# Optimization experiments

Hardware: AMD Instinct MI355X
Metric: run time of the kernel (lower is better)

The kernel has to match this reference:

```python
import jax, jax.numpy as jnp
import numpy as np

B, N, C = 1, 256, 128        # batch, n_res, norm_channel
H, AC = 4, 32                # num_head, attention_channel


def setup_inputs() -> dict:
    key = jax.random.key(0)
    ks = jax.random.split(key, 9)
    s = 0.02
    return {
        "act": jax.random.normal(ks[0], (B, N, N, C), jnp.float32),
        "mask": jnp.ones((B, N, N), jnp.float32),
        "ln_g": jnp.ones((C,), jnp.float32),
        "ln_b": jnp.zeros((C,), jnp.float32),
        "wq": (jax.random.normal(ks[1], (C, H * AC), jnp.float32) * s),
        "wk": (jax.random.normal(ks[2], (C, H * AC), jnp.float32) * s),
        "wv": (jax.random.normal(ks[3], (C, H * AC), jnp.float32) * s),
        "w2d": (jax.random.normal(ks[4], (C, H), jnp.float32) * s),
        "wg": (jax.random.normal(ks[5], (C, H * AC), jnp.float32) * s),
        "bg": jnp.zeros((H * AC,), jnp.float32),
        "wo": (jax.random.normal(ks[6], (H * AC, C), jnp.float32) * s),
        "bo": jnp.zeros((C,), jnp.float32),
    }


def reference(act, mask, ln_g, ln_b, wq, wk, wv, w2d, wg, bg, wo, bo):
    eps = 1e-5
    mu = jnp.mean(act, axis=-1, keepdims=True)
    var = jnp.mean(jnp.square(act - mu), axis=-1, keepdims=True)
    a = (act - mu) * jax.lax.rsqrt(var + eps) * ln_g + ln_b  # LayerNorm

    b_, m_, i_, _ = a.shape
    q = (a @ wq).reshape(b_, m_, i_, H, AC)
    k = (a @ wk).reshape(b_, m_, i_, H, AC)
    v = (a @ wv).reshape(b_, m_, i_, H, AC)

    factor = 1.0 / np.sqrt(AC).astype(np.float32)
    # mask bias: [b, m, 1, 1, j]
    bias = (1e9 * (mask - 1.0))[:, :, None, None, :]
    aff = jnp.einsum('bmihc,bmjhc->bmhij', q * factor, k) + bias

    # pair bias: [b, h, i, j], broadcast over m (torch trailing-dim broadcast, b=1)
    nb = jnp.einsum('bijc,ch->bhij', a, w2d)
    weights = jax.nn.softmax(aff + nb[:, None], axis=-1)  # [b,m,h,i,j]

    g = jax.nn.sigmoid(a @ wg + bg).reshape(b_, m_, i_, H, AC)
    out = jnp.einsum('bmhqk,bmkhc->bmqhc', weights, v) * g  # [b,m,q,h,c]
    return out.reshape(b_, m_, i_, H * AC) @ wo + bo
```

## Files before the change

### kernel.cpp

```cpp
#include <hip/hip_runtime.h>
#include <hip/hip_fp16.h>
#include <math.h>


#define NRES 256
#define CCH  128
#define NROWS (NRES * NRES)
#define FACTOR 0.17677669529663687f
#define LOG2E  1.44269504088896341f

typedef __attribute__((ext_vector_type(8))) __bf16 bf16x8;
typedef __attribute__((ext_vector_type(4))) float f32x4;

__device__ __forceinline__ f32x4 mfma16(bf16x8 a, bf16x8 b, f32x4 c) {
    return __builtin_amdgcn_mfma_f32_16x16x32_bf16(a, b, c, 0, 0, 0);
}

union PK4 { __bf16 b[4]; uint2 u2; };

__device__ __forceinline__ void hilo(float x, __bf16& h, __bf16& l) {
    h = (__bf16)x;
    l = (__bf16)(x - (float)h);
}

__global__ __launch_bounds__(256) void pre_kernel(
    const float* __restrict__ act, const float* __restrict__ ln_g,
    const float* __restrict__ ln_b, const float* __restrict__ w2d,
    const float* __restrict__ wq, const float* __restrict__ wk,
    const float* __restrict__ wv, const float* __restrict__ wg,
    const float* __restrict__ wo,
    __bf16* __restrict__ wph, __bf16* __restrict__ wpl,
    float* __restrict__ nbP, __bf16* __restrict__ aLN)
{
    const int t = threadIdx.x;
    if (blockIdx.x >= 2048) {
        const int gid = (blockIdx.x - 2048) * 256 + t;
        const int wid = gid >> 11;
        const int rem = gid & 2047;
        const int nstrip = rem >> 8;
        const int kf = (rem >> 6) & 3;
        const int lane = rem & 63;
        const int l15 = lane & 15, quad = lane >> 4;
        const float* W = (wid == 0) ? wq : (wid == 1) ? wk :
                         (wid == 2) ? wv : (wid == 3) ? wg : wo;
        const float scale = (wid == 0) ? FACTOR * LOG2E : 1.0f;
        bf16x8 hb, lb;
        #pragma unroll
        for (int e = 0; e < 8; ++e) {
            int k = kf * 32 + quad * 8 + e;
            int n = nstrip * 16 + l15;
            float v = W[k * CCH + n] * scale;
            __bf16 h, l; hilo(v, h, l);
            hb[e] = h; lb[e] = l;
        }
        *(bf16x8*)&wph[(size_t)gid * 8] = hb;
        *(bf16x8*)&wpl[(size_t)gid * 8] = lb;
        return;
    }
    const int ridx = t >> 3, g = t & 7;
    const int grow = blockIdx.x * 32 + ridx;
    const float* __restrict__ xp = act + (size_t)grow * CCH + g * 16;
    float4 x4[4];
    #pragma unroll
    for (int c = 0; c < 4; ++c) x4[c] = *(const float4*)(xp + c * 4);
    float s = 0.f, sq = 0.f;
    #pragma unroll
    for (int c = 0; c < 4; ++c) {
        s  += (x4[c].x + x4[c].y) + (x4[c].z + x4[c].w);
        sq += x4[c].x * x4[c].x + x4[c].y * x4[c].y +
              x4[c].z * x4[c].z + x4[c].w * x4[c].w;
    }
    #pragma unroll
    for (int o = 1; o <= 4; o <<= 1) {
        s  += __shfl_xor(s, o, 64);
        sq += __shfl_xor(sq, o, 64);
    }
    float mu  = s * (1.0f / CCH);
    float var = fmaf(sq, 1.0f / CCH, -mu * mu);
    float rs  = rsqrtf(var + 1e-5f);
    float av[16];
    #pragma unroll
    for (int c = 0; c < 4; ++c) {
        float4 g4 = *(const float4*)&ln_g[g * 16 + c * 4];
        float4 b4 = *(const float4*)&ln_b[g * 16 + c * 4];
        float* xv = (float*)&x4[c];
        float* gv = (float*)&g4;
        float* bv = (float*)&b4;
        #pragma unroll
        for (int e = 0; e < 4; ++e)
            av[c * 4 + e] = fmaf((xv[e] - mu) * rs, gv[e], bv[e]);
    }
    bf16x8 o1, o2;
    #pragma unroll
    for (int e = 0; e < 8; ++e) {
        o1[e] = (__bf16)av[e];
        o2[e] = (__bf16)av[8 + e];
    }
    *(bf16x8*)&aLN[(size_t)grow * CCH + g * 16] = o1;
    *(bf16x8*)&aLN[(size_t)grow * CCH + g * 16 + 8] = o2;

    float nb[4] = {0.f, 0.f, 0.f, 0.f};
    const float4* __restrict__ w2d4 = (const float4*)w2d;
    #pragma unroll
    for (int c = 0; c < 16; ++c) {
        float4 wv = w2d4[g * 16 + c];
        nb[0] = fmaf(av[c], wv.x, nb[0]);
        nb[1] = fmaf(av[c], wv.y, nb[1]);
        nb[2] = fmaf(av[c], wv.z, nb[2]);
        nb[3] = fmaf(av[c], wv.w, nb[3]);
    }
    #pragma unroll
    for (int o = 1; o <= 4; o <<= 1)
        #pragma unroll
        for (int hh = 0; hh < 4; ++hh)
            nb[hh] += __shfl_xor(nb[hh], o, 64);
    if (g == 0) {
        const int i = grow >> 8, j = grow & 255;
        #pragma unroll
        for (int hh = 0; hh < 4; ++hh) {
            size_t f = ((size_t)hh << 14) + ((size_t)(i >> 4) << 10) +
                       ((size_t)(j >> 4) << 6) + ((size_t)((j >> 2) & 3) << 4) +
                       (i & 15);
            nbP[f * 4 + (j & 3)] = nb[hh] * LOG2E;
        }
    }
}

__device__ __forceinline__ void proj16(const bf16x8* A0,
    const __bf16* __restrict__ Bh, int lane, f32x4* acc)
{
    #pragma unroll
    for (int n = 0; n < 8; ++n) acc[n] = (f32x4){0.f, 0.f, 0.f, 0.f};
    #pragma unroll
    for (int kf = 0; kf < 4; ++kf)
        #pragma unroll
        for (int n = 0; n < 8; ++n) {
            bf16x8 bh = *(const bf16x8*)&Bh[(size_t)((n * 4 + kf) * 64 + lane) * 8];
            acc[n] = mfma16(A0[kf], bh, acc[n]);
        }
}

__global__ __launch_bounds__(1024) void mega_kernel(
    const __bf16* __restrict__ aLN, const __bf16* __restrict__ wph,
    const __bf16* __restrict__ wpl, const float* __restrict__ bg,
    const float* __restrict__ mask, const float* __restrict__ nbP,
    const float* __restrict__ bo, float* __restrict__ out)
{
    __shared__ __align__(16) char smem[158720];
    const int t = threadIdx.x, w = t >> 6, lane = t & 63;
    const int l15 = lane & 15, quad = lane >> 4;
    const int m = blockIdx.x;
    __bf16* const Kl = (__bf16*)smem;
    __bf16* const aH = (__bf16*)(smem + w * 4352);
    __bf16* const VT = (__bf16*)(smem + 69632);
    __bf16* const ph = (__bf16*)(smem + 137216 + w * 1280);
    float*  const biasrow = (float*)(smem + 157696);

    if (t < 256)
        biasrow[t] = fmaf(1.442695e9f, mask[m * NRES + t] - 1.0f, -4.0f * LOG2E);

    bf16x8 A0[4];
    {
        const __bf16* __restrict__ ap =
            aLN + ((size_t)m * NRES + w * 16 + l15) * CCH;
        #pragma unroll
        for (int kf = 0; kf < 4; ++kf)
            A0[kf] = *(const bf16x8*)&ap[kf * 32 + quad * 8];
    }

    f32x4 acc[8];
    bf16x8 Qh[4];
    uint2  greg[4][2];

    proj16(A0, wph, lane, acc);
    {
        __bf16* const sth = aH;
        #pragma unroll
        for (int n = 0; n < 8; ++n)
            #pragma unroll
            for (int r = 0; r < 4; ++r)
                sth[(quad * 4 + r) * 136 + n * 16 + l15] = (__bf16)acc[n][r];
        #pragma unroll
        for (int h = 0; h < 4; ++h)
            Qh[h] = *(const bf16x8*)&sth[l15 * 136 + h * 32 + quad * 8];
    }

    proj16(A0, wph + 3 * 16384, lane, acc);
    {
        __half* const sthH = (__half*)aH;
        #pragma unroll
        for (int n = 0; n < 8; ++n)
            #pragma unroll
            for (int r = 0; r < 4; ++r) {
                float v = acc[n][r] + bg[n * 16 + l15];
                sthH[(quad * 4 + r) * 136 + n * 16 + l15] =
                    (__half)(1.0f / (1.0f + __expf(-v)));
            }
        #pragma unroll
        for (int h = 0; h < 4; ++h)
            #pragma unroll
            for (int c = 0; c < 2; ++c)
                greg[h][c] =
                    *(const uint2*)&sthH[l15 * 136 + h * 32 + c * 16 + quad * 4];
    }

    proj16(A0, wph + 1 * 16384, lane, acc);
    #pragma unroll
    for (int n = 0; n < 8; ++n)
        #pragma unroll
        for (int r = 0; r < 4; ++r)
            aH[(quad * 4 + r) * 136 + n * 16 + l15] = (__bf16)acc[n][r];

    proj16(A0, wph + 2 * 16384, lane, acc);
    {
        const int jcol = w * 16 + quad * 4;
        #pragma unroll
        for (int n = 0; n < 8; ++n) {
            PK4 pv;
            #pragma unroll
            for (int r = 0; r < 4; ++r) pv.b[r] = (__bf16)acc[n][r];
            *(uint2*)&VT[(n * 16 + l15) * 264 + jcol] = pv.u2;
        }
    }

    __syncthreads();

    uint2 ovh[4][2], ovl[4][2];
    #pragma unroll
    for (int h = 0; h < 4; ++h) {
        f32x4 O[2];
        O[0] = (f32x4){0.f, 0.f, 0.f, 0.f};
        O[1] = (f32x4){0.f, 0.f, 0.f, 0.f};
        float ls = 0.f;
        const int nbbase = (h * 16384 + w * 1024 + quad * 16 + l15) * 4;
        float4 nb_a[2], nb_b[2];
        #pragma unroll
        for (int js = 0; js < 2; ++js)
            nb_a[js] = *(const float4*)(nbP + nbbase + (js << 8));
        #pragma unroll 1
        for (int jb = 0; jb < NRES; jb += 32) {
            bf16x8 Kh[2];
            #pragma unroll
            for (int js = 0; js < 2; ++js)
                Kh[js] = *(const bf16x8*)&Kl[(jb + js * 16 + l15) * 136 +
                                             h * 32 + quad * 8];
            bf16x8 Vh2[2];
            #pragma unroll
            for (int c = 0; c < 2; ++c)
                Vh2[c] = *(const bf16x8*)&VT[(h * 32 + c * 16 + l15) * 264 +
                                             jb + quad * 8];
            const int jn = (jb + 32 < NRES) ? (jb >> 4) + 2 : 0;
            #pragma unroll
            for (int js = 0; js < 2; ++js)
                nb_b[js] = *(const float4*)(nbP + nbbase + ((jn + js) << 8));
            #pragma unroll
            for (int js = 0; js < 2; ++js) {
                f32x4 S = (f32x4){0.f, 0.f, 0.f, 0.f};
                S = mfma16(Kh[js], Qh[h], S);
                float4 nb4 = nb_a[js];
                float4 mb4 = *(const float4*)&biasrow[jb + js * 16 + quad * 4];
                float p0 = exp2f(S[0] + nb4.x + mb4.x);
                float p1 = exp2f(S[1] + nb4.y + mb4.y);
                float p2 = exp2f(S[2] + nb4.z + mb4.z);
                float p3 = exp2f(S[3] + nb4.w + mb4.w);
                ls += (p0 + p1) + (p2 + p3);
                PK4 hh;
                hh.b[0] = (__bf16)p0; hh.b[1] = (__bf16)p1;
                hh.b[2] = (__bf16)p2; hh.b[3] = (__bf16)p3;
                *(uint2*)&ph[l15 * 40 + js * 16 + quad * 4] = hh.u2;
            }
            bf16x8 Ph = *(const bf16x8*)&ph[l15 * 40 + quad * 8];
            #pragma unroll
            for (int c = 0; c < 2; ++c)
                O[c] = mfma16(Vh2[c], Ph, O[c]);
            nb_a[0] = nb_b[0];
            nb_a[1] = nb_b[1];
        }
        ls += __shfl_xor(ls, 16, 64);
        ls += __shfl_xor(ls, 32, 64);
        float inv = 1.0f / ls;
        #pragma unroll
        for (int c = 0; c < 2; ++c) {
            const __half* gh = (const __half*)&greg[h][c];
            PK4 hh, lo;
            #pragma unroll
            for (int r = 0; r < 4; ++r) {
                float v = O[c][r] * inv * (float)gh[r];
                __bf16 hb; __bf16 lb; hilo(v, hb, lb);
                hh.b[r] = hb; lo.b[r] = lb;
            }
            ovh[h][c] = hh.u2;
            ovl[h][c] = lo.u2;
        }
    }
    __syncthreads();

    {
        __bf16* const sth = aH;
        #pragma unroll
        for (int h = 0; h < 4; ++h)
            #pragma unroll
            for (int c = 0; c < 2; ++c)
                *(uint2*)&sth[l15 * 136 + h * 32 + c * 16 + quad * 4] = ovh[h][c];
        bf16x8 Ah0[4];
        #pragma unroll
        for (int kf = 0; kf < 4; ++kf)
            Ah0[kf] = *(const bf16x8*)&sth[l15 * 136 + kf * 32 + quad * 8];
        #pragma unroll
        for (int h = 0; h < 4; ++h)
            #pragma unroll
            for (int c = 0; c < 2; ++c)
                *(uint2*)&sth[l15 * 136 + h * 32 + c * 16 + quad * 4] = ovl[h][c];
        bf16x8 Al0[4];
        #pragma unroll
        for (int kf = 0; kf < 4; ++kf)
            Al0[kf] = *(const bf16x8*)&sth[l15 * 136 + kf * 32 + quad * 8];

        const __bf16* __restrict__ Bh = wph + (size_t)4 * 16384;
        const __bf16* __restrict__ Bl = wpl + (size_t)4 * 16384;
        #pragma unroll
        for (int n = 0; n < 8; ++n) acc[n] = (f32x4){0.f, 0.f, 0.f, 0.f};
        #pragma unroll
        for (int kf = 0; kf < 4; ++kf)
            #pragma unroll
            for (int n = 0; n < 8; ++n) {
                size_t boff = (size_t)((n * 4 + kf) * 64 + lane) * 8;
                bf16x8 bh = *(const bf16x8*)&Bh[boff];
                bf16x8 bl = *(const bf16x8*)&Bl[boff];
                acc[n] = mfma16(Ah0[kf], bh, acc[n]);
                acc[n] = mfma16(Ah0[kf], bl, acc[n]);
                acc[n] = mfma16(Al0[kf], bh, acc[n]);
            }

        const size_t rbase = (size_t)m * NRES + w * 16;
        #pragma unroll
        for (int n = 0; n < 8; ++n) {
            float b = bo[n * 16 + l15];
            #pragma unroll
            for (int r = 0; r < 4; ++r)
                out[(rbase + quad * 4 + r) * CCH + n * 16 + l15] = acc[n][r] + b;
        }
    }
}

extern "C" void kernel_launch(void* const* d_in, const int* in_sizes, int n_in,
                              void* d_out, int out_size, void* d_ws, size_t ws_size,
                              hipStream_t stream)
{
    const float* act  = (const float*)d_in[0];
    const float* mask = (const float*)d_in[1];
    const float* ln_g = (const float*)d_in[2];
    const float* ln_b = (const float*)d_in[3];
    const float* wq   = (const float*)d_in[4];
    const float* wk   = (const float*)d_in[5];
    const float* wv   = (const float*)d_in[6];
    const float* w2d  = (const float*)d_in[7];
    const float* wg   = (const float*)d_in[8];
    const float* bg   = (const float*)d_in[9];
    const float* wo   = (const float*)d_in[10];
    const float* bo   = (const float*)d_in[11];
    float* out = (float*)d_out;

    float* nbP = (float*)d_ws;
    __bf16* wph = (__bf16*)(nbP + 4 * NROWS);
    __bf16* wpl = wph + 5 * 16384;
    __bf16* aLN = wpl + 5 * 16384;

    pre_kernel<<<2088, 256, 0, stream>>>(
        act, ln_g, ln_b, w2d, wq, wk, wv, wg, wo, wph, wpl, nbP, aLN);
    mega_kernel<<<256, 1024, 0, stream>>>(
        aLN, wph, wpl, bg, mask, nbP, bo, out);
}
```

Before: 189.0 us.

## Use 16x16x16 MFMA to feed accumulators directly, removing LDS round-trips

Switches the PV product and the output projection to the 16x16x16 bf16 MFMA. That instruction's operand layout matches the accumulator layout of the previous MFMA, so probabilities and attention outputs can be fed straight from registers. This removes the per-iteration P staging through shared memory, the final __syncthreads, and the LDS transposes before the wo projection. It also drops the unused low-part weights for q/k/v/g and repacks wo for the new layout. In exchange it issues twice as many smaller MFMAs and more, narrower global loads of the weights.

```diff
diff --git a/kernel.cpp b/kernel.cpp
--- a/kernel.cpp
+++ b/kernel.cpp
@@ -11,12 +11,16 @@
 
 typedef __attribute__((ext_vector_type(8))) __bf16 bf16x8;
 typedef __attribute__((ext_vector_type(4))) float f32x4;
+typedef __attribute__((ext_vector_type(4))) short s16x4;
 
 __device__ __forceinline__ f32x4 mfma16(bf16x8 a, bf16x8 b, f32x4 c) {
     return __builtin_amdgcn_mfma_f32_16x16x32_bf16(a, b, c, 0, 0, 0);
 }
-
-union PK4 { __bf16 b[4]; uint2 u2; };
+__device__ __forceinline__ f32x4 mfma16x16(s16x4 a, s16x4 b, f32x4 c) {
+    return __builtin_amdgcn_mfma_f32_16x16x16bf16_1k(a, b, c, 0, 0, 0);
+}
+
+union PK4 { __bf16 b[4]; uint2 u2; s16x4 s4; };
 
 __device__ __forceinline__ void hilo(float x, __bf16& h, __bf16& l) {
     h = (__bf16)x;
@@ -29,7 +33,8 @@
     const float* __restrict__ wq, const float* __restrict__ wk,
     const float* __restrict__ wv, const float* __restrict__ wg,
     const float* __restrict__ wo,
-    __bf16* __restrict__ wph, __bf16* __restrict__ wpl,
+    __bf16* __restrict__ wph, __bf16* __restrict__ wo16h,
+    __bf16* __restrict__ wo16l,
     float* __restrict__ nbP, __bf16* __restrict__ aLN)
 {
     const int t = threadIdx.x;
@@ -37,24 +42,41 @@
         const int gid = (blockIdx.x - 2048) * 256 + t;
         const int wid = gid >> 11;
         const int rem = gid & 2047;
-        const int nstrip = rem >> 8;
-        const int kf = (rem >> 6) & 3;
         const int lane = rem & 63;
         const int l15 = lane & 15, quad = lane >> 4;
-        const float* W = (wid == 0) ? wq : (wid == 1) ? wk :
-                         (wid == 2) ? wv : (wid == 3) ? wg : wo;
-        const float scale = (wid == 0) ? FACTOR * LOG2E : 1.0f;
-        bf16x8 hb, lb;
-        #pragma unroll
-        for (int e = 0; e < 8; ++e) {
-            int k = kf * 32 + quad * 8 + e;
-            int n = nstrip * 16 + l15;
-            float v = W[k * CCH + n] * scale;
-            __bf16 h, l; hilo(v, h, l);
-            hb[e] = h; lb[e] = l;
-        }
-        *(bf16x8*)&wph[(size_t)gid * 8] = hb;
-        *(bf16x8*)&wpl[(size_t)gid * 8] = lb;
+        if (wid < 4) {
+            const int nstrip = rem >> 8;
+            const int kf = (rem >> 6) & 3;
+            const float* W = (wid == 0) ? wq : (wid == 1) ? wk :
+                             (wid == 2) ? wv : wg;
+            const float scale = (wid == 0) ? FACTOR * LOG2E : 1.0f;
+            bf16x8 hb;
+            #pragma unroll
+            for (int e = 0; e < 8; ++e) {
+                int k = kf * 32 + quad * 8 + e;
+                int n = nstrip * 16 + l15;
+                hb[e] = (__bf16)(W[k * CCH + n] * scale);
+            }
+            *(bf16x8*)&wph[(size_t)gid * 8] = hb;
+        } else {
+            const int nstrip = rem >> 8;
+            const int kcp = (rem >> 6) & 3;
+            #pragma unroll
+            for (int sub = 0; sub < 2; ++sub) {
+                const int kc = kcp * 2 + sub;
+                PK4 hh, ll;
+                #pragma unroll
+                for (int e = 0; e < 4; ++e) {
+                    int k = kc * 16 + quad * 4 + e;
+                    int n = nstrip * 16 + l15;
+                    __bf16 h, l; hilo(wo[k * CCH + n], h, l);
+                    hh.b[e] = h; ll.b[e] = l;
+                }
+                const int fo = ((nstrip * 8 + kc) * 64 + lane) * 4;
+                *(uint2*)&wo16h[fo] = hh.u2;
+                *(uint2*)&wo16l[fo] = ll.u2;
+            }
+        }
         return;
     }
     const int ridx = t >> 3, g = t & 7;
@@ -142,19 +164,19 @@
 
 __global__ __launch_bounds__(1024) void mega_kernel(
     const __bf16* __restrict__ aLN, const __bf16* __restrict__ wph,
-    const __bf16* __restrict__ wpl, const float* __restrict__ bg,
-    const float* __restrict__ mask, const float* __restrict__ nbP,
-    const float* __restrict__ bo, float* __restrict__ out)
+    const __bf16* __restrict__ wo16h, const __bf16* __restrict__ wo16l,
+    const float* __restrict__ bg, const float* __restrict__ mask,
+    const float* __restrict__ nbP, const float* __restrict__ bo,
+    float* __restrict__ out)
 {
-    __shared__ __align__(16) char smem[158720];
+    __shared__ __align__(16) char smem[138240];
     const int t = threadIdx.x, w = t >> 6, lane = t & 63;
     const int l15 = lane & 15, quad = lane >> 4;
     const int m = blockIdx.x;
     __bf16* const Kl = (__bf16*)smem;
     __bf16* const aH = (__bf16*)(smem + w * 4352);
     __bf16* const VT = (__bf16*)(smem + 69632);
-    __bf16* const ph = (__bf16*)(smem + 137216 + w * 1280);
-    float*  const biasrow = (float*)(smem + 157696);
+    float*  const biasrow = (float*)(smem + 137216);
 
     if (t < 256)
         biasrow[t] = fmaf(1.442695e9f, mask[m * NRES + t] - 1.0f, -4.0f * LOG2E);
@@ -225,7 +247,7 @@
 
     __syncthreads();
 
-    uint2 ovh[4][2], ovl[4][2];
+    PK4 ovh[4][2], ovl[4][2];
     #pragma unroll
     for (int h = 0; h < 4; ++h) {
         f32x4 O[2];
@@ -244,35 +266,47 @@
             for (int js = 0; js < 2; ++js)
                 Kh[js] = *(const bf16x8*)&Kl[(jb + js * 16 + l15) * 136 +
                                              h * 32 + quad * 8];
-            bf16x8 Vh2[2];
+            PK4 Vf[2][2];
             #pragma unroll
             for (int c = 0; c < 2; ++c)
-                Vh2[c] = *(const bf16x8*)&VT[(h * 32 + c * 16 + l15) * 264 +
-                                             jb + quad * 8];
+                #pragma unroll
+                for (int js = 0; js < 2; ++js)
+                    Vf[c][js].u2 = *(const uint2*)&VT[
+                        (h * 32 + c * 16 + l15) * 264 + jb + js * 16 + quad * 4];
             const int jn = (jb + 32 < NRES) ? (jb >> 4) + 2 : 0;
             #pragma unroll
             for (int js = 0; js < 2; ++js)
                 nb_b[js] = *(const float4*)(nbP + nbbase + ((jn + js) << 8));
-            #pragma unroll
-            for (int js = 0; js < 2; ++js) {
-                f32x4 S = (f32x4){0.f, 0.f, 0.f, 0.f};
-                S = mfma16(Kh[js], Qh[h], S);
-                float4 nb4 = nb_a[js];
-                float4 mb4 = *(const float4*)&biasrow[jb + js * 16 + quad * 4];
-                float p0 = exp2f(S[0] + nb4.x + mb4.x);
-                float p1 = exp2f(S[1] + nb4.y + mb4.y);
-                float p2 = exp2f(S[2] + nb4.z + mb4.z);
-                float p3 = exp2f(S[3] + nb4.w + mb4.w);
+            f32x4 S0 = (f32x4){0.f, 0.f, 0.f, 0.f};
+            f32x4 S1 = (f32x4){0.f, 0.f, 0.f, 0.f};
+            S0 = mfma16(Kh[0], Qh[h], S0);
+            S1 = mfma16(Kh[1], Qh[h], S1);
+            PK4 PJ0, PJ1;
+            {
+                float4 mb0 = *(const float4*)&biasrow[jb + quad * 4];
+                float p0 = exp2f(S0[0] + nb_a[0].x + mb0.x);
+                float p1 = exp2f(S0[1] + nb_a[0].y + mb0.y);
+                float p2 = exp2f(S0[2] + nb_a[0].z + mb0.z);
+                float p3 = exp2f(S0[3] + nb_a[0].w + mb0.w);
                 ls += (p0 + p1) + (p2 + p3);
-                PK4 hh;
-                hh.b[0] = (__bf16)p0; hh.b[1] = (__bf16)p1;
-                hh.b[2] = (__bf16)p2; hh.b[3] = (__bf16)p3;
-                *(uint2*)&ph[l15 * 40 + js * 16 + quad * 4] = hh.u2;
-            }
-            bf16x8 Ph = *(const bf16x8*)&ph[l15 * 40 + quad * 8];
-            #pragma unroll
-            for (int c = 0; c < 2; ++c)
-                O[c] = mfma16(Vh2[c], Ph, O[c]);
+                PJ0.b[0] = (__bf16)p0; PJ0.b[1] = (__bf16)p1;
+                PJ0.b[2] = (__bf16)p2; PJ0.b[3] = (__bf16)p3;
+            }
+            {
+                float4 mb1 = *(const float4*)&biasrow[jb + 16 + quad * 4];
+                float p0 = exp2f(S1[0] + nb_a[1].x + mb1.x);
+                float p1 = exp2f(S1[1] + nb_a[1].y + mb1.y);
+                float p2 = exp2f(S1[2] + nb_a[1].z + mb1.z);
+                float p3 = exp2f(S1[3] + nb_a[1].w + mb1.w);
+                ls += (p0 + p1) + (p2 + p3);
+                PJ1.b[0] = (__bf16)p0; PJ1.b[1] = (__bf16)p1;
+                PJ1.b[2] = (__bf16)p2; PJ1.b[3] = (__bf16)p3;
+            }
+            #pragma unroll
+            for (int c = 0; c < 2; ++c) {
+                O[c] = mfma16x16(Vf[c][0].s4, PJ0.s4, O[c]);
+                O[c] = mfma16x16(Vf[c][1].s4, PJ1.s4, O[c]);
+            }
             nb_a[0] = nb_b[0];
             nb_a[1] = nb_b[1];
         }
@@ -282,55 +316,34 @@
         #pragma unroll
         for (int c = 0; c < 2; ++c) {
             const __half* gh = (const __half*)&greg[h][c];
-            PK4 hh, lo;
             #pragma unroll
             for (int r = 0; r < 4; ++r) {
                 float v = O[c][r] * inv * (float)gh[r];
                 __bf16 hb; __bf16 lb; hilo(v, hb, lb);
-                hh.b[r] = hb; lo.b[r] = lb;
-            }
-            ovh[h][c] = hh.u2;
-            ovl[h][c] = lo.u2;
-        }
-    }
-    __syncthreads();
-
-    {
-        __bf16* const sth = aH;
-        #pragma unroll
-        for (int h = 0; h < 4; ++h)
-            #pragma unroll
-            for (int c = 0; c < 2; ++c)
-                *(uint2*)&sth[l15 * 136 + h * 32 + c * 16 + quad * 4] = ovh[h][c];
-        bf16x8 Ah0[4];
-        #pragma unroll
-        for (int kf = 0; kf < 4; ++kf)
-            Ah0[kf] = *(const bf16x8*)&sth[l15 * 136 + kf * 32 + quad * 8];
-        #pragma unroll
-        for (int h = 0; h < 4; ++h)
-            #pragma unroll
-            for (int c = 0; c < 2; ++c)
-                *(uint2*)&sth[l15 * 136 + h * 32 + c * 16 + quad * 4] = ovl[h][c];
-        bf16x8 Al0[4];
-        #pragma unroll
-        for (int kf = 0; kf < 4; ++kf)
-            Al0[kf] = *(const bf16x8*)&sth[l15 * 136 + kf * 32 + quad * 8];
-
-        const __bf16* __restrict__ Bh = wph + (size_t)4 * 16384;
-        const __bf16* __restrict__ Bl = wpl + (size_t)4 * 16384;
+                ovh[h][c].b[r] = hb; ovl[h][c].b[r] = lb;
+            }
+        }
+    }
+
+    {
         #pragma unroll
         for (int n = 0; n < 8; ++n) acc[n] = (f32x4){0.f, 0.f, 0.f, 0.f};
         #pragma unroll
-        for (int kf = 0; kf < 4; ++kf)
+        for (int kc = 0; kc < 8; ++kc) {
+            const int h = kc >> 1, c = kc & 1;
+            s16x4 Ah = ovh[h][c].s4;
+            s16x4 Al = ovl[h][c].s4;
             #pragma unroll
             for (int n = 0; n < 8; ++n) {
-                size_t boff = (size_t)((n * 4 + kf) * 64 + lane) * 8;
-                bf16x8 bh = *(const bf16x8*)&Bh[boff];
-                bf16x8 bl = *(const bf16x8*)&Bl[boff];
-                acc[n] = mfma16(Ah0[kf], bh, acc[n]);
-                acc[n] = mfma16(Ah0[kf], bl, acc[n]);
-                acc[n] = mfma16(Al0[kf], bh, acc[n]);
-            }
+                const int fo = ((n * 8 + kc) * 64 + lane) * 4;
+                PK4 bh, bl;
+                bh.u2 = *(const uint2*)&wo16h[fo];
+                bl.u2 = *(const uint2*)&wo16l[fo];
+                acc[n] = mfma16x16(Ah, bh.s4, acc[n]);
+                acc[n] = mfma16x16(Ah, bl.s4, acc[n]);
+                acc[n] = mfma16x16(Al, bh.s4, acc[n]);
+            }
+        }
 
         const size_t rbase = (size_t)m * NRES + w * 16;
         #pragma unroll
@@ -361,13 +374,14 @@
     const float* bo   = (const float*)d_in[11];
     float* out = (float*)d_out;
 
-    float* nbP = (float*)d_ws;
-    __bf16* wph = (__bf16*)(nbP + 4 * NROWS);
-    __bf16* wpl = wph + 5 * 16384;
-    __bf16* aLN = wpl + 5 * 16384;
+    float* nbP    = (float*)d_ws;
+    __bf16* wph   = (__bf16*)(nbP + 4 * NROWS);
+    __bf16* wo16h = wph + 4 * 16384;
+    __bf16* wo16l = wo16h + 16384;
+    __bf16* aLN   = wo16l + 16384;
 
     pre_kernel<<<2088, 256, 0, stream>>>(
-        act, ln_g, ln_b, w2d, wq, wk, wv, wg, wo, wph, wpl, nbP, aLN);
+        act, ln_g, ln_b, w2d, wq, wk, wv, wg, wo, wph, wo16h, wo16l, nbP, aLN);
     mega_kernel<<<256, 1024, 0, stream>>>(
-        aLN, wph, wpl, bg, mask, nbP, bo, out);
-}
+        aLN, wph, wo16h, wo16l, bg, mask, nbP, bo, out);
+}
```

Result: faster. 185.1 us (-2.1%).
